# Optimization experiments

Hardware: AMD Instinct MI355X
Metric: run time of the kernel (lower is better)

## Reference

```python
import jax, jax.numpy as jnp
import numpy as np

N = 50000      # nodes
F_IN = 128     # in_features
F_OUT = 128    # out_features
E = 800000     # edges (avg degree 16)


def setup_inputs() -> dict:
    key = jax.random.key(0)
    k = jax.random.split(key, 6)
    x = jax.random.normal(k[0], (N, F_IN), dtype=jnp.float32)
    h0 = jax.random.normal(k[1], (N, F_IN), dtype=jnp.float32)
    edge_row = jax.random.randint(k[2], (E,), 0, N, dtype=jnp.int32)
    edge_col = jax.random.randint(k[3], (E,), 0, N, dtype=jnp.int32)
    # normalized-Laplacian-like positive weights
    edge_val = jax.random.uniform(k[4], (E,), dtype=jnp.float32)
    stdv = 1.0 / np.sqrt(F_OUT)
    weight = jax.random.uniform(k[5], (F_IN, F_OUT), dtype=jnp.float32,
                                minval=-stdv, maxval=stdv)
    return {
        "input": x,
        "h0": h0,
        "edge_row": edge_row,
        "edge_col": edge_col,
        "edge_val": edge_val,
        "weight": weight,
        "lamda": jnp.float32(0.5),
        "alpha": jnp.float32(0.1),
        "l": 4,  # layer index (python int)
    }


def reference(input, h0, edge_row, edge_col, edge_val, weight, lamda, alpha, l):
    # theta = log(lamda / l + 1)
    theta = jnp.log(lamda / l + 1.0)
    # hi = spmm(G, input): gather source features, scale by edge value, scatter-add to rows
    msgs = edge_val[:, None] * input[edge_col]              # [E, F]
    hi = jax.ops.segment_sum(msgs, edge_row, num_segments=N)  # [N, F]
    # variant=False: support == r == (1-alpha)*hi + alpha*h0
    support = (1.0 - alpha) * hi + alpha * h0
    out = theta * (support @ weight) + (1.0 - theta) * support
    # residual=True
    out = out + input
    return out
```

## Files before the change

kernel.cpp:

```cpp
#include <hip/hip_runtime.h>
#include <math.h>

#define NF 128
#define SCAN_B 1024

typedef __bf16 bf16x8 __attribute__((ext_vector_type(8)));
typedef float  f32x4  __attribute__((ext_vector_type(4)));


__device__ __forceinline__ unsigned short f2bf(float f) {
    unsigned int u = __float_as_uint(f);
    u = (u + 0x7fffu + ((u >> 16) & 1u)) >> 16;
    return (unsigned short)u;
}
__device__ __forceinline__ float bf2f(unsigned short s) {
    return __uint_as_float((unsigned int)s << 16);
}

__global__ __launch_bounds__(256) void cvt_kernel(
    const float* __restrict__ x, uint* __restrict__ xb, int n8) {
    int i = blockIdx.x * 256 + threadIdx.x;
    if (i >= n8) return;
    float4 a = ((const float4*)x)[i * 2];
    float4 b = ((const float4*)x)[i * 2 + 1];
    uint4 o;
    o.x = (uint)f2bf(a.x) | ((uint)f2bf(a.y) << 16);
    o.y = (uint)f2bf(a.z) | ((uint)f2bf(a.w) << 16);
    o.z = (uint)f2bf(b.x) | ((uint)f2bf(b.y) << 16);
    o.w = (uint)f2bf(b.z) | ((uint)f2bf(b.w) << 16);
    ((uint4*)xb)[i] = o;
}

__global__ __launch_bounds__(256) void cvtW_kernel(
    const float* __restrict__ W, unsigned short* __restrict__ Wt) {
    int idx = blockIdx.x * 256 + threadIdx.x;
    int k = idx >> 7, n = idx & 127;
    Wt[n * NF + k] = f2bf(W[k * NF + n]);
}


__global__ __launch_bounds__(256) void hist_kernel(
    const int* __restrict__ erow, int* __restrict__ cnt, int E_) {
    int e = blockIdx.x * 256 + threadIdx.x;
    if (e < E_) atomicAdd(&cnt[erow[e]], 1);
}

__global__ __launch_bounds__(SCAN_B) void scanA_kernel(
    const int* __restrict__ cnt, int* __restrict__ bsum, int N_) {
    __shared__ int buf[SCAN_B];
    int t = threadIdx.x;
    int i = blockIdx.x * SCAN_B + t;
    buf[t] = (i < N_) ? cnt[i] : 0;
    __syncthreads();
    for (int d = SCAN_B / 2; d > 0; d >>= 1) {
        if (t < d) buf[t] += buf[t + d];
        __syncthreads();
    }
    if (t == 0) bsum[blockIdx.x] = buf[0];
}

__global__ __launch_bounds__(SCAN_B) void scanC_kernel(
    const int* __restrict__ cnt, const int* __restrict__ bsum,
    int* __restrict__ off, int* __restrict__ pos, int N_, int nb) {
    __shared__ int buf[SCAN_B];
    __shared__ int bpre_sh;
    int t = threadIdx.x;
    if (t < 64) {
        int v0 = (t < nb) ? bsum[t] : 0;
        int v = v0;
        for (int d = 1; d < 64; d <<= 1) {
            int u = __shfl_up(v, d, 64);
            if (t >= d) v += u;
        }
        if (t == (int)blockIdx.x) bpre_sh = v - v0;
        if (blockIdx.x == 0 && t == nb - 1) off[N_] = v;
    }
    int i = blockIdx.x * SCAN_B + t;
    int v = (i < N_) ? cnt[i] : 0;
    buf[t] = v;
    __syncthreads();
    for (int d = 1; d < SCAN_B; d <<= 1) {
        int add = (t >= d) ? buf[t - d] : 0;
        __syncthreads();
        buf[t] += add;
        __syncthreads();
    }
    if (i < N_) {
        int o = bpre_sh + buf[t] - v;
        off[i] = o;
        pos[i] = o;
    }
}

__global__ __launch_bounds__(256) void fill_kernel(
    const int* __restrict__ erow, const int* __restrict__ ecol,
    const float* __restrict__ evalv, int* __restrict__ pos,
    int2* __restrict__ epack, int E_) {
    int e = blockIdx.x * 256 + threadIdx.x;
    if (e >= E_) return;
    int p = atomicAdd(&pos[erow[e]], 1);
    int2 pk;
    pk.x = ecol[e];
    pk.y = __float_as_int(evalv[e]);
    epack[p] = pk;
}


#define UNPK_FMA(u, v, a0, a1)                         \
    a0 += (v) * __uint_as_float((u) << 16);            \
    a1 += (v) * __uint_as_float((u) & 0xffff0000u);

__global__ __launch_bounds__(256) void spmm_kernel(
    const unsigned short* __restrict__ xb, const float* __restrict__ h0,
    const int* __restrict__ off, const int2* __restrict__ epack,
    unsigned short* __restrict__ supb, const float* __restrict__ alpha_p, int N_) {
    int w = (blockIdx.x * 256 + threadIdx.x) >> 6;
    if (w >= N_) return;
    int lane = threadIdx.x & 63;
    int g    = lane >> 4;
    int seg  = lane & 15;
    int s = off[w], e = off[w + 1];
    float acc[8] = {};
    int i = s + g;
    for (; i + 4 < e; i += 8) {
        int2 e0 = epack[i];
        int2 e1 = epack[i + 4];
        float v0 = __int_as_float(e0.y);
        float v1 = __int_as_float(e1.y);
        uint4 a = *(const uint4*)(xb + (size_t)e0.x * NF + seg * 8);
        uint4 b = *(const uint4*)(xb + (size_t)e1.x * NF + seg * 8);
        UNPK_FMA(a.x, v0, acc[0], acc[1]);
        UNPK_FMA(a.y, v0, acc[2], acc[3]);
        UNPK_FMA(a.z, v0, acc[4], acc[5]);
        UNPK_FMA(a.w, v0, acc[6], acc[7]);
        UNPK_FMA(b.x, v1, acc[0], acc[1]);
        UNPK_FMA(b.y, v1, acc[2], acc[3]);
        UNPK_FMA(b.z, v1, acc[4], acc[5]);
        UNPK_FMA(b.w, v1, acc[6], acc[7]);
    }
    if (i < e) {
        int2 e0 = epack[i];
        float v0 = __int_as_float(e0.y);
        uint4 a = *(const uint4*)(xb + (size_t)e0.x * NF + seg * 8);
        UNPK_FMA(a.x, v0, acc[0], acc[1]);
        UNPK_FMA(a.y, v0, acc[2], acc[3]);
        UNPK_FMA(a.z, v0, acc[4], acc[5]);
        UNPK_FMA(a.w, v0, acc[6], acc[7]);
    }
#pragma unroll
    for (int j = 0; j < 8; j++) {
        acc[j] += __shfl_xor(acc[j], 16, 64);
        acc[j] += __shfl_xor(acc[j], 32, 64);
    }
    if (g == 0) {
        float alpha = *alpha_p;
        float oma = 1.0f - alpha;
        const float* h = h0 + (size_t)w * NF + seg * 8;
        float4 ha = *(const float4*)h;
        float4 hb = *(const float4*)(h + 4);
        float o0 = oma * acc[0] + alpha * ha.x;
        float o1 = oma * acc[1] + alpha * ha.y;
        float o2 = oma * acc[2] + alpha * ha.z;
        float o3 = oma * acc[3] + alpha * ha.w;
        float o4 = oma * acc[4] + alpha * hb.x;
        float o5 = oma * acc[5] + alpha * hb.y;
        float o6 = oma * acc[6] + alpha * hb.z;
        float o7 = oma * acc[7] + alpha * hb.w;
        uint4 pk;
        pk.x = (uint)f2bf(o0) | ((uint)f2bf(o1) << 16);
        pk.y = (uint)f2bf(o2) | ((uint)f2bf(o3) << 16);
        pk.z = (uint)f2bf(o4) | ((uint)f2bf(o5) << 16);
        pk.w = (uint)f2bf(o6) | ((uint)f2bf(o7) << 16);
        *(uint4*)(supb + (size_t)w * NF + seg * 8) = pk;
    }
}


__global__ __launch_bounds__(256) void gemm_mfma_kernel(
    const unsigned short* __restrict__ supb, const unsigned short* __restrict__ Wt,
    const float* __restrict__ x, float* __restrict__ out,
    const float* __restrict__ lamda_p, const int* __restrict__ l_p, int n_rows) {
    int wave = threadIdx.x >> 6;
    int lane = threadIdx.x & 63;
    int m0 = blockIdx.x * 64 + wave * 16;
    if (m0 >= n_rows) return;

    float theta = logf((*lamda_p) / (float)(*l_p) + 1.0f);
    float omt = 1.0f - theta;

    int lr = lane & 15;
    int kg = lane >> 4;

    bf16x8 afr[4];
    const unsigned short* abase = supb + (size_t)(m0 + lr) * NF + kg * 8;
#pragma unroll
    for (int kt = 0; kt < 4; kt++)
        afr[kt] = *reinterpret_cast<const bf16x8*>(abase + kt * 32);

#pragma unroll
    for (int nt = 0; nt < 8; nt++) {
        int n0 = nt * 16;
        const unsigned short* bbase = Wt + (size_t)(n0 + lr) * NF + kg * 8;
        f32x4 acc = {0.f, 0.f, 0.f, 0.f};
#pragma unroll
        for (int kt = 0; kt < 4; kt++) {
            bf16x8 bfr = *reinterpret_cast<const bf16x8*>(bbase + kt * 32);
            acc = __builtin_amdgcn_mfma_f32_16x16x32_bf16(afr[kt], bfr, acc, 0, 0, 0);
        }
        int ncol = n0 + lr;
#pragma unroll
        for (int j = 0; j < 4; j++) {
            int m = m0 + kg * 4 + j;
            float sv = bf2f(supb[(size_t)m * NF + ncol]);
            float xv = x[(size_t)m * NF + ncol];
            out[(size_t)m * NF + ncol] = theta * acc[j] + omt * sv + xv;
        }
    }
}

extern "C" void kernel_launch(void* const* d_in, const int* in_sizes, int n_in,
                              void* d_out, int out_size, void* d_ws, size_t ws_size,
                              hipStream_t stream) {
    const float* x       = (const float*)d_in[0];
    const float* h0      = (const float*)d_in[1];
    const int*   erow    = (const int*)d_in[2];
    const int*   ecol    = (const int*)d_in[3];
    const float* evalv   = (const float*)d_in[4];
    const float* W       = (const float*)d_in[5];
    const float* lamda_p = (const float*)d_in[6];
    const float* alpha_p = (const float*)d_in[7];
    const int*   l_p     = (const int*)d_in[8];

    int N_ = in_sizes[0] / NF;
    int E_ = in_sizes[2];
    int nb = (N_ + SCAN_B - 1) / SCAN_B;

    char* ws = (char*)d_ws;
    size_t o = 0;
    auto alloc = [&](size_t bytes) { char* p = ws + o; o = (o + bytes + 255) & ~(size_t)255; return p; };
    unsigned short* supb = (unsigned short*)alloc((size_t)N_ * NF * 2);
    unsigned short* xb   = (unsigned short*)alloc((size_t)N_ * NF * 2);
    unsigned short* Wt   = (unsigned short*)alloc((size_t)NF * NF * 2);
    int*   cnt   = (int*)  alloc((size_t)N_ * sizeof(int));
    int*   off   = (int*)  alloc((size_t)(N_ + 1) * sizeof(int));
    int*   pos   = (int*)  alloc((size_t)N_ * sizeof(int));
    int2*  epack = (int2*) alloc((size_t)E_ * sizeof(int2));
    int*   bsum  = (int*)  alloc((size_t)nb * sizeof(int));

    float* out = (float*)d_out;

    int n8 = N_ * NF / 8;
    cvt_kernel<<<(n8 + 255) / 256, 256, 0, stream>>>(x, (uint*)xb, n8);
    cvtW_kernel<<<NF * NF / 256, 256, 0, stream>>>(W, Wt);

    hipMemsetAsync(cnt, 0, (size_t)N_ * sizeof(int), stream);
    hist_kernel<<<(E_ + 255) / 256, 256, 0, stream>>>(erow, cnt, E_);
    scanA_kernel<<<nb, SCAN_B, 0, stream>>>(cnt, bsum, N_);
    scanC_kernel<<<nb, SCAN_B, 0, stream>>>(cnt, bsum, off, pos, N_, nb);
    fill_kernel<<<(E_ + 255) / 256, 256, 0, stream>>>(erow, ecol, evalv, pos, epack, E_);

    int blocks = (N_ * 64 + 255) / 256;
    spmm_kernel<<<blocks, 256, 0, stream>>>(xb, h0, off, epack, supb, alpha_p, N_);

    gemm_mfma_kernel<<<(N_ + 63) / 64, 256, 0, stream>>>(
        supb, Wt, x, out, lamda_p, l_p, N_);
}
```

Measured before the change: 261.0 us.

## Fuse preprocessing and CSR build kernels into one cooperative kernel with grid syncs

Merges the bf16 conversions, memset, histogram, two-pass scan and CSR fill into one cooperative kernel of 1024 blocks, separated by grid-wide barriers. This removes six kernel launches plus a memset and the gaps between them. The scan now runs with 256-thread blocks, each thread handling four elements. In exchange it depends on cooperative launch residency, and grid.sync adds its own barrier cost. The fixed 64-entry bsum limits it to about 65k nodes.

```diff
diff --git a/kernel.cpp b/kernel.cpp
--- a/kernel.cpp
+++ b/kernel.cpp
@@ -1,8 +1,10 @@
 #include <hip/hip_runtime.h>
+#include <hip/hip_cooperative_groups.h>
 #include <math.h>
 
+namespace cg = cooperative_groups;
+
 #define NF 128
-#define SCAN_B 1024
 
 typedef __bf16 bf16x8 __attribute__((ext_vector_type(8)));
 typedef float  f32x4  __attribute__((ext_vector_type(4)));
@@ -17,54 +19,63 @@
     return __uint_as_float((unsigned int)s << 16);
 }
 
-__global__ __launch_bounds__(256) void cvt_kernel(
-    const float* __restrict__ x, uint* __restrict__ xb, int n8) {
-    int i = blockIdx.x * 256 + threadIdx.x;
-    if (i >= n8) return;
-    float4 a = ((const float4*)x)[i * 2];
-    float4 b = ((const float4*)x)[i * 2 + 1];
-    uint4 o;
-    o.x = (uint)f2bf(a.x) | ((uint)f2bf(a.y) << 16);
-    o.y = (uint)f2bf(a.z) | ((uint)f2bf(a.w) << 16);
-    o.z = (uint)f2bf(b.x) | ((uint)f2bf(b.y) << 16);
-    o.w = (uint)f2bf(b.z) | ((uint)f2bf(b.w) << 16);
-    ((uint4*)xb)[i] = o;
-}
-
-__global__ __launch_bounds__(256) void cvtW_kernel(
-    const float* __restrict__ W, unsigned short* __restrict__ Wt) {
-    int idx = blockIdx.x * 256 + threadIdx.x;
-    int k = idx >> 7, n = idx & 127;
-    Wt[n * NF + k] = f2bf(W[k * NF + n]);
-}
-
-
-__global__ __launch_bounds__(256) void hist_kernel(
-    const int* __restrict__ erow, int* __restrict__ cnt, int E_) {
-    int e = blockIdx.x * 256 + threadIdx.x;
-    if (e < E_) atomicAdd(&cnt[erow[e]], 1);
-}
-
-__global__ __launch_bounds__(SCAN_B) void scanA_kernel(
-    const int* __restrict__ cnt, int* __restrict__ bsum, int N_) {
-    __shared__ int buf[SCAN_B];
+
+__global__ __launch_bounds__(256) void build_kernel(
+    const float* __restrict__ x, const float* __restrict__ W,
+    const int* __restrict__ erow, const int* __restrict__ ecol,
+    const float* __restrict__ evalv,
+    uint* __restrict__ xb, unsigned short* __restrict__ Wt,
+    int* __restrict__ cnt, int* __restrict__ bsum,
+    int* __restrict__ off, int* __restrict__ pos, int2* __restrict__ epack,
+    int N_, int E_, int nb, int n8)
+{
+    cg::grid_group grid = cg::this_grid();
     int t = threadIdx.x;
-    int i = blockIdx.x * SCAN_B + t;
-    buf[t] = (i < N_) ? cnt[i] : 0;
-    __syncthreads();
-    for (int d = SCAN_B / 2; d > 0; d >>= 1) {
-        if (t < d) buf[t] += buf[t + d];
-        __syncthreads();
-    }
-    if (t == 0) bsum[blockIdx.x] = buf[0];
-}
-
-__global__ __launch_bounds__(SCAN_B) void scanC_kernel(
-    const int* __restrict__ cnt, const int* __restrict__ bsum,
-    int* __restrict__ off, int* __restrict__ pos, int N_, int nb) {
-    __shared__ int buf[SCAN_B];
-    __shared__ int bpre_sh;
-    int t = threadIdx.x;
+    int gtid = blockIdx.x * 256 + t;
+    int G = gridDim.x * 256;
+
+    __shared__ int sbuf[256];
+    __shared__ int pre[64];
+
+    for (int i = gtid; i < N_; i += G) cnt[i] = 0;
+    for (int i = gtid; i < n8; i += G) {
+        float4 a = ((const float4*)x)[i * 2];
+        float4 b = ((const float4*)x)[i * 2 + 1];
+        uint4 o;
+        o.x = (uint)f2bf(a.x) | ((uint)f2bf(a.y) << 16);
+        o.y = (uint)f2bf(a.z) | ((uint)f2bf(a.w) << 16);
+        o.z = (uint)f2bf(b.x) | ((uint)f2bf(b.y) << 16);
+        o.w = (uint)f2bf(b.z) | ((uint)f2bf(b.w) << 16);
+        ((uint4*)xb)[i] = o;
+    }
+    for (int i = gtid; i < NF * NF; i += G) {
+        int k = i >> 7, n = i & 127;
+        Wt[n * NF + k] = f2bf(W[k * NF + n]);
+    }
+    grid.sync();
+
+    for (int e = gtid; e < E_; e += G) atomicAdd(&cnt[erow[e]], 1);
+    grid.sync();
+
+    for (int c = blockIdx.x; c < nb; c += gridDim.x) {
+        int base_i = c * 1024 + t * 4;
+        int s = 0;
+#pragma unroll
+        for (int j = 0; j < 4; j++) {
+            int idx = base_i + j;
+            s += (idx < N_) ? cnt[idx] : 0;
+        }
+        sbuf[t] = s;
+        __syncthreads();
+        for (int d = 128; d > 0; d >>= 1) {
+            if (t < d) sbuf[t] += sbuf[t + d];
+            __syncthreads();
+        }
+        if (t == 0) bsum[c] = sbuf[0];
+        __syncthreads();
+    }
+    grid.sync();
+
     if (t < 64) {
         int v0 = (t < nb) ? bsum[t] : 0;
         int v = v0;
@@ -72,37 +83,49 @@
             int u = __shfl_up(v, d, 64);
             if (t >= d) v += u;
         }
-        if (t == (int)blockIdx.x) bpre_sh = v - v0;
-        if (blockIdx.x == 0 && t == nb - 1) off[N_] = v;
-    }
-    int i = blockIdx.x * SCAN_B + t;
-    int v = (i < N_) ? cnt[i] : 0;
-    buf[t] = v;
+        pre[t] = v - v0;
+    }
     __syncthreads();
-    for (int d = 1; d < SCAN_B; d <<= 1) {
-        int add = (t >= d) ? buf[t - d] : 0;
-        __syncthreads();
-        buf[t] += add;
-        __syncthreads();
-    }
-    if (i < N_) {
-        int o = bpre_sh + buf[t] - v;
-        off[i] = o;
-        pos[i] = o;
-    }
-}
-
-__global__ __launch_bounds__(256) void fill_kernel(
-    const int* __restrict__ erow, const int* __restrict__ ecol,
-    const float* __restrict__ evalv, int* __restrict__ pos,
-    int2* __restrict__ epack, int E_) {
-    int e = blockIdx.x * 256 + threadIdx.x;
-    if (e >= E_) return;
-    int p = atomicAdd(&pos[erow[e]], 1);
-    int2 pk;
-    pk.x = ecol[e];
-    pk.y = __float_as_int(evalv[e]);
-    epack[p] = pk;
+    for (int c = blockIdx.x; c < nb; c += gridDim.x) {
+        int base_i = c * 1024 + t * 4;
+        int v[4];
+        int s = 0;
+#pragma unroll
+        for (int j = 0; j < 4; j++) {
+            int idx = base_i + j;
+            v[j] = (idx < N_) ? cnt[idx] : 0;
+            s += v[j];
+        }
+        sbuf[t] = s;
+        __syncthreads();
+        for (int d = 1; d < 256; d <<= 1) {
+            int add = (t >= d) ? sbuf[t - d] : 0;
+            __syncthreads();
+            sbuf[t] += add;
+            __syncthreads();
+        }
+        int base = pre[c] + sbuf[t] - s;
+#pragma unroll
+        for (int j = 0; j < 4; j++) {
+            int idx = base_i + j;
+            if (idx < N_) {
+                off[idx] = base;
+                pos[idx] = base;
+                base += v[j];
+            }
+        }
+        __syncthreads();
+    }
+    if (blockIdx.x == 0 && t == 0) off[N_] = pre[nb - 1] + bsum[nb - 1];
+    grid.sync();
+
+    for (int e = gtid; e < E_; e += G) {
+        int p = atomicAdd(&pos[erow[e]], 1);
+        int2 pk;
+        pk.x = ecol[e];
+        pk.y = __float_as_int(evalv[e]);
+        epack[p] = pk;
+    }
 }
 
 
@@ -233,7 +256,8 @@
 
     int N_ = in_sizes[0] / NF;
     int E_ = in_sizes[2];
-    int nb = (N_ + SCAN_B - 1) / SCAN_B;
+    int nb = (N_ + 1023) / 1024;
+    int n8 = N_ * NF / 8;
 
     char* ws = (char*)d_ws;
     size_t o = 0;
@@ -245,19 +269,19 @@
     int*   off   = (int*)  alloc((size_t)(N_ + 1) * sizeof(int));
     int*   pos   = (int*)  alloc((size_t)N_ * sizeof(int));
     int2*  epack = (int2*) alloc((size_t)E_ * sizeof(int2));
-    int*   bsum  = (int*)  alloc((size_t)nb * sizeof(int));
+    int*   bsum  = (int*)  alloc(64 * sizeof(int));
 
     float* out = (float*)d_out;
 
-    int n8 = N_ * NF / 8;
-    cvt_kernel<<<(n8 + 255) / 256, 256, 0, stream>>>(x, (uint*)xb, n8);
-    cvtW_kernel<<<NF * NF / 256, 256, 0, stream>>>(W, Wt);
-
-    hipMemsetAsync(cnt, 0, (size_t)N_ * sizeof(int), stream);
-    hist_kernel<<<(E_ + 255) / 256, 256, 0, stream>>>(erow, cnt, E_);
-    scanA_kernel<<<nb, SCAN_B, 0, stream>>>(cnt, bsum, N_);
-    scanC_kernel<<<nb, SCAN_B, 0, stream>>>(cnt, bsum, off, pos, N_, nb);
-    fill_kernel<<<(E_ + 255) / 256, 256, 0, stream>>>(erow, ecol, evalv, pos, epack, E_);
+    uint* xbu = (uint*)xb;
+    void* args[] = {
+        (void*)&x, (void*)&W, (void*)&erow, (void*)&ecol, (void*)&evalv,
+        (void*)&xbu, (void*)&Wt, (void*)&cnt, (void*)&bsum,
+        (void*)&off, (void*)&pos, (void*)&epack,
+        (void*)&N_, (void*)&E_, (void*)&nb, (void*)&n8
+    };
+    hipLaunchCooperativeKernel((void*)build_kernel, dim3(1024), dim3(256),
+                               args, 0, stream);
 
     int blocks = (N_ * 64 + 255) / 256;
     spmm_kernel<<<blocks, 256, 0, stream>>>(xb, h0, off, epack, supb, alpha_p, N_);
```

After: 661.1 us. 2.53x slower.
